# Kernel tuning notes

Hardware: AMD Instinct MI355X
Metric: run time of the kernel (lower is better)

The kernel has to match this reference:

```python
import jax, jax.numpy as jnp
import numpy as np

NUM_RAYS = 262144   # 512x512 rays
LENGTH = 128        # path_length
NUM_LEAVES = 1048576
MAX_DIST = 1e10
EPS = 1e-10


def setup_inputs() -> dict:
    key = jax.random.key(0)
    k1, k2, k3 = jax.random.split(key, 3)
    # t_stops must be increasing along each ray
    t_stops = jnp.sort(jax.random.uniform(k1, (NUM_RAYS, LENGTH), jnp.float32, 0.0, 4.0), axis=-1)
    leaves = jax.random.randint(k2, (NUM_RAYS, LENGTH), 0, NUM_LEAVES, dtype=jnp.int64)
    logits = jax.random.normal(k3, (NUM_LEAVES,), jnp.float32) - 10.0  # init near -10 like the module
    return {"t_stops": t_stops, "leaves": leaves, "logits": logits}


def reference(t_stops, leaves, logits):
    num_rays, length = leaves.shape
    # gather per-sample opacity
    opacity = jax.nn.sigmoid(logits)[leaves]                      # [R, L]
    # segment lengths; last segment extends to "infinity"
    deltas = jnp.concatenate(
        [t_stops[:, 1:] - t_stops[:, :-1],
         jnp.full((num_rays, 1), MAX_DIST, dtype=t_stops.dtype)], axis=-1)
    alpha = 1.0 - jnp.exp(-(opacity * deltas))                    # [R, L]
    trans = jnp.minimum(1.0, 1.0 - alpha + EPS)
    # shift right: transmittance before first sample is 1
    trans = jnp.concatenate(
        [jnp.ones((num_rays, 1), dtype=alpha.dtype), trans[:, 1:]], axis=-1)
    weights = alpha * jnp.cumprod(trans, axis=-1)                 # [R, L]
    return weights.sum(axis=-1)                                   # [R]
```

## Files before the change

kernel.cpp:

```cpp
#include <hip/hip_runtime.h>
#include <math.h>


#define NRAYS 262144
#define LEN   128
#define MAXD  1e10f
#define EPSW  1e-10f

__global__ __launch_bounds__(256) void vc_kernel(
    const float* __restrict__ t_stops,
    const int*   __restrict__ leaves,
    const float* __restrict__ logits,
    float*       __restrict__ out)
{
    const int lane = threadIdx.x & 63;
    const int wave = threadIdx.x >> 6;
    const int ray  = blockIdx.x * 4 + wave;

    const long long base = (long long)ray * LEN + 2 * lane;

    float2 t2 = *(const float2*)(t_stops + base);
    int2   lv = *(const int2*)(leaves + base);

    float t_next = __shfl_down(t2.x, 1);
    float d0 = t2.y - t2.x;
    float d1 = (lane == 63) ? MAXD : (t_next - t2.y);

    float lg0 = logits[lv.x];
    float lg1 = logits[lv.y];
    float op0 = 1.0f / (1.0f + expf(-lg0));
    float op1 = 1.0f / (1.0f + expf(-lg1));

    float a0 = -expm1f(-op0 * d0);
    float a1 = -expm1f(-op1 * d1);

    float tr0 = fminf(1.0f, 1.0f - a0 + EPSW);
    float tr1 = fminf(1.0f, 1.0f - a1 + EPSW);
    if (lane == 0) tr0 = 1.0f;

    float p01 = tr0 * tr1;

    float scan = p01;
    #pragma unroll
    for (int off = 1; off < 64; off <<= 1) {
        float v = __shfl_up(scan, off);
        if (lane >= off) scan *= v;
    }
    float excl = __shfl_up(scan, 1);
    if (lane == 0) excl = 1.0f;

    float w = a0 * (excl * tr0) + a1 * (excl * p01);

    #pragma unroll
    for (int off = 32; off >= 1; off >>= 1)
        w += __shfl_xor(w, off);

    if (lane == 0)
        out[ray] = w;
}

extern "C" void kernel_launch(void* const* d_in, const int* in_sizes, int n_in,
                              void* d_out, int out_size, void* d_ws, size_t ws_size,
                              hipStream_t stream) {
    const float* t_stops = (const float*)d_in[0];
    const int*   leaves  = (const int*)d_in[1];
    const float* logits  = (const float*)d_in[2];
    float*       out     = (float*)d_out;

    dim3 grid(NRAYS / 4), block(256);
    vc_kernel<<<grid, block, 0, stream>>>(t_stops, leaves, logits, out);
}
```

Baseline: 424.4 us.

## Process two rays per wave with float4 loads and associative compositing reduction

Each wave now handles two rays, with 32 lanes per ray and four samples per lane loaded as float4/int4. The separate prefix-product scan and sum reduction are replaced by one butterfly reduction over (transmittance product, weighted sum) pairs, so the shuffle rounds drop from about twelve to ten combined steps. Sigmoid and 1-exp(-x) now use a fast reciprocal, __expf and a small-x polynomial, which trims transcendental cost at some cost in precision. The kernel is likely dominated by the random logits gather, so the gain is bounded.

```diff
diff --git a/kernel.cpp b/kernel.cpp
--- a/kernel.cpp
+++ b/kernel.cpp
@@ -7,6 +7,16 @@
 #define MAXD  1e10f
 #define EPSW  1e-10f
 
+__device__ __forceinline__ float fast_sigmoid(float x) {
+    return __builtin_amdgcn_rcpf(1.0f + __expf(-x));
+}
+
+__device__ __forceinline__ float one_minus_exp_neg(float x) {
+    float poly = x * (1.0f + x * (-0.5f + x * (0.16666667f - 0.041666668f * x)));
+    float big  = 1.0f - __expf(-x);
+    return (x < 0.1f) ? poly : big;
+}
+
 __global__ __launch_bounds__(256) void vc_kernel(
     const float* __restrict__ t_stops,
     const int*   __restrict__ leaves,
@@ -14,49 +24,54 @@
     float*       __restrict__ out)
 {
     const int lane = threadIdx.x & 63;
-    const int wave = threadIdx.x >> 6;
-    const int ray  = blockIdx.x * 4 + wave;
+    const int wid  = blockIdx.x * 4 + (threadIdx.x >> 6);
+    const int ray  = wid * 2 + (lane >> 5);
+    const int sub  = lane & 31;
 
-    const long long base = (long long)ray * LEN + 2 * lane;
+    const long long base = (long long)ray * LEN + sub * 4;
 
-    float2 t2 = *(const float2*)(t_stops + base);
-    int2   lv = *(const int2*)(leaves + base);
+    float4 t4 = *(const float4*)(t_stops + base);
+    int4   lv = *(const int4*)(leaves + base);
 
-    float t_next = __shfl_down(t2.x, 1);
-    float d0 = t2.y - t2.x;
-    float d1 = (lane == 63) ? MAXD : (t_next - t2.y);
+    float tnext = __shfl_down(t4.x, 1);
+    float d0 = t4.y - t4.x;
+    float d1 = t4.z - t4.y;
+    float d2 = t4.w - t4.z;
+    float d3 = (sub == 31) ? MAXD : (tnext - t4.w);
 
-    float lg0 = logits[lv.x];
-    float lg1 = logits[lv.y];
-    float op0 = 1.0f / (1.0f + expf(-lg0));
-    float op1 = 1.0f / (1.0f + expf(-lg1));
+    float x0 = fast_sigmoid(logits[lv.x]) * d0;
+    float x1 = fast_sigmoid(logits[lv.y]) * d1;
+    float x2 = fast_sigmoid(logits[lv.z]) * d2;
+    float x3 = fast_sigmoid(logits[lv.w]) * d3;
 
-    float a0 = -expm1f(-op0 * d0);
-    float a1 = -expm1f(-op1 * d1);
+    float a0 = one_minus_exp_neg(x0);
+    float a1 = one_minus_exp_neg(x1);
+    float a2 = one_minus_exp_neg(x2);
+    float a3 = one_minus_exp_neg(x3);
 
     float tr0 = fminf(1.0f, 1.0f - a0 + EPSW);
     float tr1 = fminf(1.0f, 1.0f - a1 + EPSW);
-    if (lane == 0) tr0 = 1.0f;
+    float tr2 = fminf(1.0f, 1.0f - a2 + EPSW);
+    float tr3 = fminf(1.0f, 1.0f - a3 + EPSW);
+    if (sub == 0) tr0 = 1.0f;
 
-    float p01 = tr0 * tr1;
-
-    float scan = p01;
-    #pragma unroll
-    for (int off = 1; off < 64; off <<= 1) {
-        float v = __shfl_up(scan, off);
-        if (lane >= off) scan *= v;
-    }
-    float excl = __shfl_up(scan, 1);
-    if (lane == 0) excl = 1.0f;
-
-    float w = a0 * (excl * tr0) + a1 * (excl * p01);
+    float c = tr0;
+    float S = a0 * c;
+    c *= tr1;  S = fmaf(a1, c, S);
+    c *= tr2;  S = fmaf(a2, c, S);
+    c *= tr3;  S = fmaf(a3, c, S);
+    float P = c;
 
     #pragma unroll
-    for (int off = 32; off >= 1; off >>= 1)
-        w += __shfl_xor(w, off);
+    for (int o = 1; o < 32; o <<= 1) {
+        float Pp = __shfl_xor(P, o);
+        float Sp = __shfl_xor(S, o);
+        S = (lane & o) ? fmaf(Pp, S, Sp) : fmaf(P, Sp, S);
+        P *= Pp;
+    }
 
-    if (lane == 0)
-        out[ray] = w;
+    if (sub == 0)
+        out[ray] = S;
 }
 
 extern "C" void kernel_launch(void* const* d_in, const int* in_sizes, int n_in,
@@ -67,6 +82,6 @@
     const float* logits  = (const float*)d_in[2];
     float*       out     = (float*)d_out;
 
-    dim3 grid(NRAYS / 4), block(256);
+    dim3 grid(NRAYS / 8), block(256);
     vc_kernel<<<grid, block, 0, stream>>>(t_stops, leaves, logits, out);
 }
```

Result: faster. 410.1 us (-3.4%).
